# Kernel tuning notes

Measured on AMD Instinct MI355X. Metric: run time of the kernel, lower is better.

The kernel has to match this reference:

```python
import jax, jax.numpy as jnp
import numpy as np

N = 50000
E = 800000
IN_DIM = 256
HID = 64
HEADS = 4
OUT_DIM = 32
NEG_SLOPE = 0.2


def gat_conv(x, edge_index, W, a_src, a_dst, bias, heads, out_ch, concat):
    """PyG-style GATConv (eval mode, add_self_loops=True).
    x: [N, F_in]; edge_index: [2, E'] with row0=src, row1=dst.
    W: [F_in, heads*out_ch]; a_src/a_dst: [heads, out_ch]; bias: [heads*out_ch] or [out_ch].
    """
    n = x.shape[0]
    # add self loops
    loops = jnp.arange(n, dtype=edge_index.dtype)
    src = jnp.concatenate([edge_index[0], loops])
    dst = jnp.concatenate([edge_index[1], loops])

    h = (x @ W).reshape(n, heads, out_ch)              # [N, H, C]
    alpha_s = jnp.einsum('nhc,hc->nh', h, a_src)       # [N, H]
    alpha_d = jnp.einsum('nhc,hc->nh', h, a_dst)       # [N, H]
    e = alpha_s[src] + alpha_d[dst]                    # [E', H]
    e = jnp.where(e >= 0, e, NEG_SLOPE * e)            # leaky_relu

    # segment softmax over incoming edges of each dst node
    m = jax.ops.segment_max(e, dst, num_segments=n)    # [N, H]
    ex = jnp.exp(e - m[dst])
    denom = jax.ops.segment_sum(ex, dst, num_segments=n)
    alpha = ex / (denom[dst] + 1e-16)                  # [E', H]

    msg = h[src] * alpha[:, :, None]                   # [E', H, C]
    out = jax.ops.segment_sum(msg, dst, num_segments=n)  # [N, H, C]
    out = out.reshape(n, heads * out_ch) if concat else out.mean(axis=1)
    return out + bias


def setup_inputs() -> dict:
    key = jax.random.key(0)
    ks = jax.random.split(key, 10)
    x = jax.random.normal(ks[0], (N, IN_DIM), dtype=jnp.float32)
    edge_index = jax.random.randint(ks[1], (2, E), 0, N, dtype=jnp.int32)
    s1 = 1.0 / np.sqrt(IN_DIM)
    s2 = 1.0 / np.sqrt(HEADS * HID)
    return {
        'x': x,
        'edge_index': edge_index,
        'W1': jax.random.normal(ks[2], (IN_DIM, HEADS * HID), dtype=jnp.float32) * s1,
        'a_src1': jax.random.normal(ks[3], (HEADS, HID), dtype=jnp.float32) * s2,
        'a_dst1': jax.random.normal(ks[4], (HEADS, HID), dtype=jnp.float32) * s2,
        'b1': jnp.zeros((HEADS * HID,), dtype=jnp.float32),
        'W2': jax.random.normal(ks[5], (HEADS * HID, OUT_DIM), dtype=jnp.float32) * s2,
        'a_src2': jax.random.normal(ks[6], (1, OUT_DIM), dtype=jnp.float32) * 0.125,
        'a_dst2': jax.random.normal(ks[7], (1, OUT_DIM), dtype=jnp.float32) * 0.125,
        'b2': jnp.zeros((OUT_DIM,), dtype=jnp.float32),
    }


def reference(x, edge_index, W1, a_src1, a_dst1, b1, W2, a_src2, a_dst2, b2):
    h = gat_conv(x, edge_index, W1, a_src1, a_dst1, b1, HEADS, HID, concat=True)
    h = jax.nn.elu(h)
    out = gat_conv(h, edge_index, W2, a_src2, a_dst2, b2, 1, OUT_DIM, concat=False)
    return out
```

## Files before the change

### kernel.cpp

```cpp
#include <hip/hip_runtime.h>

#define NEG_SLOPE 0.2f
#define CAP 64
#define LOG2E 1.44269504f

typedef short bf16x8 __attribute__((ext_vector_type(8)));
typedef float f32x4 __attribute__((ext_vector_type(4)));
typedef _Float16 half2v __attribute__((ext_vector_type(2)));
typedef _Float16 half4v __attribute__((ext_vector_type(4)));
typedef _Float16 half8v __attribute__((ext_vector_type(8)));

__device__ inline short bf16_rne(float x) {
    unsigned u = __float_as_uint(x);
    unsigned r = u + 0x7FFFu + ((u >> 16) & 1u);
    return (short)(r >> 16);
}

__device__ inline float fast_exp2(float x) {
#if __has_builtin(__builtin_amdgcn_exp2f)
    return __builtin_amdgcn_exp2f(x);
#else
    return exp2f(x);
#endif
}


__global__ void k_prepw(const float* __restrict__ W1, short* __restrict__ Wt,
                        const float* __restrict__ W2, _Float16* __restrict__ W2t,
                        int* __restrict__ cursor, int* __restrict__ col, int N) {
    int colc = blockIdx.x;
    int k = threadIdx.x;
    Wt[(size_t)colc * 256 + k] = bf16_rne(W1[(size_t)k * 256 + colc]);
    if (colc < 32) W2t[(size_t)colc * 256 + k] = (_Float16)W2[(size_t)k * 32 + colc];
    int gid = blockIdx.x * 256 + threadIdx.x;
    if (gid < N) {
        cursor[gid] = 1;
        col[(size_t)gid * CAP] = gid;
    }
}


__global__ __launch_bounds__(256) void k_gemm_scatter(
        const float* __restrict__ x, const short* __restrict__ Wt,
        const float* __restrict__ a_src, const float* __restrict__ a_dst,
        _Float16* __restrict__ h1, float* __restrict__ as1, float* __restrict__ ad1,
        int N, int nGemm,
        const int* __restrict__ srcI, const int* __restrict__ dstI,
        int* __restrict__ cursor, int* __restrict__ col, int E) {
    __shared__ short Ab[64 * 40];
    __shared__ short Bb[256 * 40];

    if ((int)blockIdx.x >= nGemm) {
        int i = ((int)blockIdx.x - nGemm) * 256 + threadIdx.x;
        if (i < E) {
            int d = dstI[i];
            int p = atomicAdd(&cursor[d], 1);
            if (p < CAP) col[(size_t)d * CAP + p] = srcI[i];
        }
        return;
    }

    const int tid = threadIdx.x;
    const int lane = tid & 63;
    const int wc = tid >> 6;
    const int row0 = blockIdx.x * 64;
    const int m15 = lane & 15, quad = lane >> 4;

    f32x4 acc[4][4] = {};

    const int arow = tid >> 2;
    const int akseg = (tid & 3) * 8;

    for (int k0 = 0; k0 < 256; k0 += 32) {
        {
            int row = row0 + arow;
            float vals[8];
            if (row < N) {
                float4 v0 = *(const float4*)(x + (size_t)row * 256 + k0 + akseg);
                float4 v1 = *(const float4*)(x + (size_t)row * 256 + k0 + akseg + 4);
                vals[0] = v0.x; vals[1] = v0.y; vals[2] = v0.z; vals[3] = v0.w;
                vals[4] = v1.x; vals[5] = v1.y; vals[6] = v1.z; vals[7] = v1.w;
            } else {
#pragma unroll
                for (int i = 0; i < 8; ++i) vals[i] = 0.f;
            }
            short buf[8];
#pragma unroll
            for (int i = 0; i < 8; ++i) buf[i] = bf16_rne(vals[i]);
            *(bf16x8*)&Ab[arow * 40 + akseg] = *(bf16x8*)&buf[0];
        }
        {
#pragma unroll
            for (int s = 0; s < 4; ++s)
                *(bf16x8*)&Bb[tid * 40 + s * 8] =
                    *(const bf16x8*)(Wt + (size_t)tid * 256 + k0 + s * 8);
        }
        __syncthreads();
        bf16x8 ab[4];
#pragma unroll
        for (int mt = 0; mt < 4; ++mt)
            ab[mt] = *(const bf16x8*)&Ab[(mt * 16 + m15) * 40 + quad * 8];
#pragma unroll
        for (int nt = 0; nt < 4; ++nt) {
            int nn = wc * 64 + nt * 16 + m15;
            bf16x8 bb = *(const bf16x8*)&Bb[nn * 40 + quad * 8];
#pragma unroll
            for (int mt = 0; mt < 4; ++mt)
                acc[mt][nt] = __builtin_amdgcn_mfma_f32_16x16x32_bf16(ab[mt], bb, acc[mt][nt], 0, 0, 0);
        }
        __syncthreads();
    }
    const int head = wc;
#pragma unroll
    for (int mt = 0; mt < 4; ++mt) {
        float va[4] = {0.f, 0.f, 0.f, 0.f};
        float vd[4] = {0.f, 0.f, 0.f, 0.f};
#pragma unroll
        for (int nt = 0; nt < 4; ++nt) {
            int colg = wc * 64 + nt * 16 + m15;
            float asv = a_src[colg];
            float adv = a_dst[colg];
#pragma unroll
            for (int r = 0; r < 4; ++r) {
                float accv = acc[mt][nt][r];
                int row = row0 + mt * 16 + quad * 4 + r;
                if (row < N) h1[(size_t)row * 256 + colg] = (_Float16)accv;
                va[r] = fmaf(accv, asv, va[r]);
                vd[r] = fmaf(accv, adv, vd[r]);
            }
        }
#pragma unroll
        for (int r = 0; r < 4; ++r) {
#pragma unroll
            for (int mq = 1; mq < 16; mq <<= 1) {
                va[r] += __shfl_xor(va[r], mq);
                vd[r] += __shfl_xor(vd[r], mq);
            }
            int row = row0 + mt * 16 + quad * 4 + r;
            if (m15 == 0 && row < N) {
                as1[(size_t)row * 4 + head] = va[r] * LOG2E;
                ad1[(size_t)row * 4 + head] = vd[r] * LOG2E;
            }
        }
    }
}


__global__ __launch_bounds__(256) void k_fuse1(
        const _Float16* __restrict__ h1, const float* __restrict__ as1,
        const float* __restrict__ ad1, const int* __restrict__ cursor,
        const int* __restrict__ col, const float* __restrict__ b1,
        const _Float16* __restrict__ W2t, const float* __restrict__ a_s2,
        const float* __restrict__ a_d2, _Float16* __restrict__ z,
        float* __restrict__ as2, float* __restrict__ ad2, int N) {
    __shared__ _Float16 W2s[32 * 264];
    __shared__ _Float16 h2s[4 * 256];
    const int tid = threadIdx.x;
    const int l = tid & 63;
    const int wave = tid >> 6;
    const int n = blockIdx.x * 4 + wave;

    for (int i8 = tid; i8 < 1024; i8 += 256) {
        int elem = i8 * 8;
        int row = elem >> 8, k = elem & 255;
        *(half8v*)&W2s[row * 264 + k] = *(const half8v*)(W2t + (size_t)row * 256 + k);
    }
    __syncthreads();
    if (n >= N) return;

    const int head = l >> 4;
    const int beg = n * CAP;
    int deg = __builtin_amdgcn_readfirstlane(cursor[n]);
    if (deg > CAP) deg = CAP;
    int colv = 0;
    if (l < deg) colv = col[beg + l];
    float adv = ad1[(size_t)n * 4 + head];

    f32x4 a0 = {}, a1 = {}, a2 = {}, a3 = {};
    float s0 = 0.f, s1 = 0.f, s2 = 0.f, s3 = 0.f;
    int j = 0;
    for (; j + 3 < deg; j += 4) {
        int c0 = __builtin_amdgcn_readlane(colv, j);
        int c1 = __builtin_amdgcn_readlane(colv, j + 1);
        int c2 = __builtin_amdgcn_readlane(colv, j + 2);
        int c3 = __builtin_amdgcn_readlane(colv, j + 3);
        float e0 = as1[(size_t)c0 * 4 + head] + adv;
        float e1 = as1[(size_t)c1 * 4 + head] + adv;
        float e2 = as1[(size_t)c2 * 4 + head] + adv;
        float e3 = as1[(size_t)c3 * 4 + head] + adv;
        e0 = fmaxf(e0, NEG_SLOPE * e0); e1 = fmaxf(e1, NEG_SLOPE * e1);
        e2 = fmaxf(e2, NEG_SLOPE * e2); e3 = fmaxf(e3, NEG_SLOPE * e3);
        float p0 = fast_exp2(e0), p1 = fast_exp2(e1);
        float p2 = fast_exp2(e2), p3 = fast_exp2(e3);
        half4v h0 = *((const half4v*)(h1 + (size_t)c0 * 256) + l);
        half4v hv1 = *((const half4v*)(h1 + (size_t)c1 * 256) + l);
        half4v h2 = *((const half4v*)(h1 + (size_t)c2 * 256) + l);
        half4v h3 = *((const half4v*)(h1 + (size_t)c3 * 256) + l);
        s0 += p0; s1 += p1; s2 += p2; s3 += p3;
        a0 += __builtin_convertvector(h0, f32x4) * p0;
        a1 += __builtin_convertvector(hv1, f32x4) * p1;
        a2 += __builtin_convertvector(h2, f32x4) * p2;
        a3 += __builtin_convertvector(h3, f32x4) * p3;
    }
    for (; j < deg; ++j) {
        int c0 = __builtin_amdgcn_readlane(colv, j);
        float e0 = as1[(size_t)c0 * 4 + head] + adv;
        e0 = fmaxf(e0, NEG_SLOPE * e0);
        float p0 = fast_exp2(e0);
        half4v h0 = *((const half4v*)(h1 + (size_t)c0 * 256) + l);
        s0 += p0;
        a0 += __builtin_convertvector(h0, f32x4) * p0;
    }
    f32x4 at = (a0 + a1) + (a2 + a3);
    float iv = 1.f / ((s0 + s1) + (s2 + s3) + 1e-16f);
    float4 bb = *(const float4*)(b1 + l * 4);
    float4 v;
    v.x = at[0] * iv + bb.x;
    v.y = at[1] * iv + bb.y;
    v.z = at[2] * iv + bb.z;
    v.w = at[3] * iv + bb.w;
    v.x = (v.x > 0.f) ? v.x : (__expf(v.x) - 1.f);
    v.y = (v.y > 0.f) ? v.y : (__expf(v.y) - 1.f);
    v.z = (v.z > 0.f) ? v.z : (__expf(v.z) - 1.f);
    v.w = (v.w > 0.f) ? v.w : (__expf(v.w) - 1.f);
    half4v hv;
    hv.x = (_Float16)v.x; hv.y = (_Float16)v.y; hv.z = (_Float16)v.z; hv.w = (_Float16)v.w;
    *((half4v*)(h2s + wave * 256) + l) = hv;

    int c = l & 31;
    int kh = (l >> 5) * 128;
    const _Float16* hrow = h2s + wave * 256 + kh;
    const _Float16* wrow = W2s + c * 264 + kh;
    float accz = 0.f;
#pragma unroll
    for (int k = 0; k < 128; k += 8) {
        half8v hz = *(const half8v*)(hrow + k);
        half8v wz = *(const half8v*)(wrow + k);
#if __has_builtin(__builtin_amdgcn_fdot2)
        accz = __builtin_amdgcn_fdot2(__builtin_shufflevector(hz, hz, 0, 1),
                                      __builtin_shufflevector(wz, wz, 0, 1), accz, false);
        accz = __builtin_amdgcn_fdot2(__builtin_shufflevector(hz, hz, 2, 3),
                                      __builtin_shufflevector(wz, wz, 2, 3), accz, false);
        accz = __builtin_amdgcn_fdot2(__builtin_shufflevector(hz, hz, 4, 5),
                                      __builtin_shufflevector(wz, wz, 4, 5), accz, false);
        accz = __builtin_amdgcn_fdot2(__builtin_shufflevector(hz, hz, 6, 7),
                                      __builtin_shufflevector(wz, wz, 6, 7), accz, false);
#else
        accz = fmaf((float)hz[0], (float)wz[0], accz);
        accz = fmaf((float)hz[1], (float)wz[1], accz);
        accz = fmaf((float)hz[2], (float)wz[2], accz);
        accz = fmaf((float)hz[3], (float)wz[3], accz);
        accz = fmaf((float)hz[4], (float)wz[4], accz);
        accz = fmaf((float)hz[5], (float)wz[5], accz);
        accz = fmaf((float)hz[6], (float)wz[6], accz);
        accz = fmaf((float)hz[7], (float)wz[7], accz);
#endif
    }
    accz += __shfl_xor(accz, 32);
    float za = accz * a_s2[c];
    float zd = accz * a_d2[c];
#pragma unroll
    for (int mq = 1; mq < 32; mq <<= 1) {
        za += __shfl_xor(za, mq);
        zd += __shfl_xor(zd, mq);
    }
    if (l < 32) z[(size_t)n * 32 + c] = (_Float16)accz;
    if (l == 0) {
        as2[n] = za * LOG2E;
        ad2[n] = zd * LOG2E;
    }
}


__global__ void k_gather2(const _Float16* __restrict__ z, const float* __restrict__ as2,
                          const float* __restrict__ ad2, const int* __restrict__ cursor,
                          const int* __restrict__ col, const float* __restrict__ b2,
                          float* __restrict__ out, int N) {
    int n = blockIdx.x * 4 + (threadIdx.x >> 6);
    if (n >= N) return;
    int l = threadIdx.x & 63;
    int eo = l >> 3;
    int cg = l & 7;
    int beg = n * CAP;
    int deg = __builtin_amdgcn_readfirstlane(cursor[n]);
    if (deg > CAP) deg = CAP;
    int colv = 0;
    if (l < deg) colv = col[beg + l];
    float adn = ad2[n];
    f32x4 acc = {};
    float s = 0.f;

    const int nst = (deg + 7) >> 3;
    int srcA = __shfl(colv, eo);
    float aA = as2[srcA];
    half4v zA = *((const half4v*)(z + (size_t)srcA * 32) + cg);
    for (int t = 0; t < nst; ++t) {
        int srcB = 0; float aB = 0.f; half4v zB = {};
        if (t + 1 < nst) {
            srcB = __shfl(colv, (t + 1) * 8 + eo);
            aB = as2[srcB];
            zB = *((const half4v*)(z + (size_t)srcB * 32) + cg);
        }
        float e = aA + adn;
        e = fmaxf(e, NEG_SLOPE * e);
        float p = (t * 8 + eo < deg) ? fast_exp2(e) : 0.f;
        s += p;
        acc += __builtin_convertvector(zA, f32x4) * p;
        srcA = srcB; aA = aB; zA = zB;
    }
    float ax = acc[0], ay = acc[1], az = acc[2], aw = acc[3];
#pragma unroll
    for (int mq = 8; mq < 64; mq <<= 1) {
        ax += __shfl_xor(ax, mq);
        ay += __shfl_xor(ay, mq);
        az += __shfl_xor(az, mq);
        aw += __shfl_xor(aw, mq);
        s += __shfl_xor(s, mq);
    }
    if (eo == 0) {
        float iv = 1.f / (s + 1e-16f);
        float4 bb = *(const float4*)(b2 + cg * 4);
        float4 v;
        v.x = ax * iv + bb.x;
        v.y = ay * iv + bb.y;
        v.z = az * iv + bb.z;
        v.w = aw * iv + bb.w;
        *(float4*)(out + (size_t)n * 32 + cg * 4) = v;
    }
}


extern "C" void kernel_launch(void* const* d_in, const int* in_sizes, int n_in,
                              void* d_out, int out_size, void* d_ws, size_t ws_size,
                              hipStream_t stream) {
    const float* x    = (const float*)d_in[0];
    const int*   ei   = (const int*)d_in[1];
    const float* W1   = (const float*)d_in[2];
    const float* a_s1 = (const float*)d_in[3];
    const float* a_d1 = (const float*)d_in[4];
    const float* b1   = (const float*)d_in[5];
    const float* W2   = (const float*)d_in[6];
    const float* a_s2 = (const float*)d_in[7];
    const float* a_d2 = (const float*)d_in[8];
    const float* b2   = (const float*)d_in[9];
    float* out = (float*)d_out;

    const int N = in_sizes[0] / 256;
    const int E = in_sizes[1] / 2;
    const int* srcIdx = ei;
    const int* dstIdx = ei + E;

    char* ws = (char*)d_ws;
    size_t off = 0;
    auto alloc = [&](size_t bytes) {
        void* p = ws + off;
        off += (bytes + 255) & ~(size_t)255;
        return p;
    };
    _Float16* h1   = (_Float16*)alloc((size_t)N * 256 * 2);
    _Float16* z    = (_Float16*)alloc((size_t)N * 32 * 2);
    float* as1    = (float*)alloc((size_t)N * 16);
    float* ad1    = (float*)alloc((size_t)N * 16);
    float* as2    = (float*)alloc((size_t)N * 4);
    float* ad2    = (float*)alloc((size_t)N * 4);
    short* Wt     = (short*)alloc((size_t)256 * 256 * 2);
    _Float16* W2t = (_Float16*)alloc((size_t)32 * 256 * 2);
    int*   cursor = (int*)alloc((size_t)N * 4);
    int*   col    = (int*)alloc((size_t)N * CAP * 4);

    k_prepw<<<256, 256, 0, stream>>>(W1, Wt, W2, W2t, cursor, col, N);

    const int nGemm = (N + 63) / 64;
    const int nScat = (E + 255) / 256;
    k_gemm_scatter<<<nGemm + nScat, 256, 0, stream>>>(
        x, Wt, a_s1, a_d1, h1, as1, ad1, N, nGemm, srcIdx, dstIdx, cursor, col, E);

    k_fuse1<<<(N + 3) / 4, 256, 0, stream>>>(h1, as1, ad1, cursor, col, b1, W2t,
                                             a_s2, a_d2, z, as2, ad2, N);

    k_gather2<<<(N + 3) / 4, 256, 0, stream>>>(z, as2, ad2, cursor, col, b2, out, N);
}
```

Baseline: 262.0 us.

## Split scatter from GEMM kernel and pad per-node atomic cursors to separate lines

Moves the edge-scatter CSR build out of the combined GEMM/scatter launch into its own kernel that runs before the first-layer GEMM. It also spaces each node's atomic cursor 16 ints (64 bytes) apart, so concurrent atomics on different destination nodes hit different cache lines instead of contending on shared ones. The cost is a larger, sparser cursor array that later kernels read with strided loads, plus an extra kernel launch and the loss of overlap between the scatter and GEMM work.

```diff
diff --git a/kernel.cpp b/kernel.cpp
--- a/kernel.cpp
+++ b/kernel.cpp
@@ -2,6 +2,7 @@
 
 #define NEG_SLOPE 0.2f
 #define CAP 64
+#define CSTRIDE 16
 #define LOG2E 1.44269504f
 
 typedef short bf16x8 __attribute__((ext_vector_type(8)));
@@ -34,32 +35,29 @@
     if (colc < 32) W2t[(size_t)colc * 256 + k] = (_Float16)W2[(size_t)k * 32 + colc];
     int gid = blockIdx.x * 256 + threadIdx.x;
     if (gid < N) {
-        cursor[gid] = 1;
+        cursor[(size_t)gid * CSTRIDE] = 1;
         col[(size_t)gid * CAP] = gid;
     }
 }
 
 
-__global__ __launch_bounds__(256) void k_gemm_scatter(
+__global__ void k_scatter(const int* __restrict__ src, const int* __restrict__ dst,
+                          int* cursor, int* col, int E) {
+    int i = blockIdx.x * 256 + threadIdx.x;
+    if (i < E) {
+        int d = dst[i];
+        int p = atomicAdd(&cursor[(size_t)d * CSTRIDE], 1);
+        if (p < CAP) col[(size_t)d * CAP + p] = src[i];
+    }
+}
+
+
+__global__ __launch_bounds__(256) void k_gemm1(
         const float* __restrict__ x, const short* __restrict__ Wt,
         const float* __restrict__ a_src, const float* __restrict__ a_dst,
-        _Float16* __restrict__ h1, float* __restrict__ as1, float* __restrict__ ad1,
-        int N, int nGemm,
-        const int* __restrict__ srcI, const int* __restrict__ dstI,
-        int* __restrict__ cursor, int* __restrict__ col, int E) {
+        _Float16* __restrict__ h1, float* __restrict__ as1, float* __restrict__ ad1, int N) {
     __shared__ short Ab[64 * 40];
     __shared__ short Bb[256 * 40];
-
-    if ((int)blockIdx.x >= nGemm) {
-        int i = ((int)blockIdx.x - nGemm) * 256 + threadIdx.x;
-        if (i < E) {
-            int d = dstI[i];
-            int p = atomicAdd(&cursor[d], 1);
-            if (p < CAP) col[(size_t)d * CAP + p] = srcI[i];
-        }
-        return;
-    }
-
     const int tid = threadIdx.x;
     const int lane = tid & 63;
     const int wc = tid >> 6;
@@ -170,7 +168,7 @@
 
     const int head = l >> 4;
     const int beg = n * CAP;
-    int deg = __builtin_amdgcn_readfirstlane(cursor[n]);
+    int deg = __builtin_amdgcn_readfirstlane(cursor[(size_t)n * CSTRIDE]);
     if (deg > CAP) deg = CAP;
     int colv = 0;
     if (l < deg) colv = col[beg + l];
@@ -282,7 +280,7 @@
     int eo = l >> 3;
     int cg = l & 7;
     int beg = n * CAP;
-    int deg = __builtin_amdgcn_readfirstlane(cursor[n]);
+    int deg = __builtin_amdgcn_readfirstlane(cursor[(size_t)n * CSTRIDE]);
     if (deg > CAP) deg = CAP;
     int colv = 0;
     if (l < deg) colv = col[beg + l];
@@ -365,15 +363,13 @@
     float* ad2    = (float*)alloc((size_t)N * 4);
     short* Wt     = (short*)alloc((size_t)256 * 256 * 2);
     _Float16* W2t = (_Float16*)alloc((size_t)32 * 256 * 2);
-    int*   cursor = (int*)alloc((size_t)N * 4);
+    int*   cursor = (int*)alloc((size_t)N * CSTRIDE * 4);
     int*   col    = (int*)alloc((size_t)N * CAP * 4);
 
     k_prepw<<<256, 256, 0, stream>>>(W1, Wt, W2, W2t, cursor, col, N);
-
-    const int nGemm = (N + 63) / 64;
-    const int nScat = (E + 255) / 256;
-    k_gemm_scatter<<<nGemm + nScat, 256, 0, stream>>>(
-        x, Wt, a_s1, a_d1, h1, as1, ad1, N, nGemm, srcIdx, dstIdx, cursor, col, E);
+    k_scatter<<<(E + 255) / 256, 256, 0, stream>>>(srcIdx, dstIdx, cursor, col, E);
+
+    k_gemm1<<<(N + 63) / 64, 256, 0, stream>>>(x, Wt, a_s1, a_d1, h1, as1, ad1, N);
 
     k_fuse1<<<(N + 3) / 4, 256, 0, stream>>>(h1, as1, ad1, cursor, col, b1, W2t,
                                              a_s2, a_d2, z, as2, ad2, N);
```

Result: no change. 266.6 us (+1.7%).

## Interleave edge scatter inside GEMM blocks, alternating before and after the GEMM

Applied to the files above, without the earlier changes.

Drops the separate scatter-only blocks. Each of the GEMM blocks now also handles a contiguous chunk of the edge list, with odd blocks scattering before the GEMM and even blocks after it. The goal is to overlap the atomic-heavy, latency-bound scatter with compute-bound MFMA work inside the same CUs and to shrink the grid. The cost is longer per-block runtimes, a strided loop over about 1000 edges per block, and register pressure shared between the two phases.

```diff
diff --git a/kernel.cpp b/kernel.cpp
--- a/kernel.cpp
+++ b/kernel.cpp
@@ -6,7 +6,6 @@
 
 typedef short bf16x8 __attribute__((ext_vector_type(8)));
 typedef float f32x4 __attribute__((ext_vector_type(4)));
-typedef _Float16 half2v __attribute__((ext_vector_type(2)));
 typedef _Float16 half4v __attribute__((ext_vector_type(4)));
 typedef _Float16 half8v __attribute__((ext_vector_type(8)));
 
@@ -40,30 +39,34 @@
 }
 
 
-__global__ __launch_bounds__(256) void k_gemm_scatter(
+__global__ __launch_bounds__(256) void k_gemm1_scatter(
         const float* __restrict__ x, const short* __restrict__ Wt,
         const float* __restrict__ a_src, const float* __restrict__ a_dst,
-        _Float16* __restrict__ h1, float* __restrict__ as1, float* __restrict__ ad1,
-        int N, int nGemm,
+        _Float16* __restrict__ h1, float* __restrict__ as1, float* __restrict__ ad1, int N,
         const int* __restrict__ srcI, const int* __restrict__ dstI,
         int* __restrict__ cursor, int* __restrict__ col, int E) {
     __shared__ short Ab[64 * 40];
     __shared__ short Bb[256 * 40];
-
-    if ((int)blockIdx.x >= nGemm) {
-        int i = ((int)blockIdx.x - nGemm) * 256 + threadIdx.x;
-        if (i < E) {
+    const int tid = threadIdx.x;
+    const int b = blockIdx.x;
+    const int nGemm = gridDim.x;
+
+    const int chunk = (E + nGemm - 1) / nGemm;
+    const int ss = b * chunk;
+    const int se = (ss + chunk < E) ? (ss + chunk) : E;
+    const bool scatterFirst = (b & 1);
+
+    if (scatterFirst) {
+        for (int i = ss + tid; i < se; i += 256) {
             int d = dstI[i];
             int p = atomicAdd(&cursor[d], 1);
             if (p < CAP) col[(size_t)d * CAP + p] = srcI[i];
         }
-        return;
-    }
-
-    const int tid = threadIdx.x;
+    }
+
     const int lane = tid & 63;
     const int wc = tid >> 6;
-    const int row0 = blockIdx.x * 64;
+    const int row0 = b * 64;
     const int m15 = lane & 15, quad = lane >> 4;
 
     f32x4 acc[4][4] = {};
@@ -141,6 +144,14 @@
                 as1[(size_t)row * 4 + head] = va[r] * LOG2E;
                 ad1[(size_t)row * 4 + head] = vd[r] * LOG2E;
             }
+        }
+    }
+
+    if (!scatterFirst) {
+        for (int i = ss + tid; i < se; i += 256) {
+            int d = dstI[i];
+            int p = atomicAdd(&cursor[d], 1);
+            if (p < CAP) col[(size_t)d * CAP + p] = srcI[i];
         }
     }
 }
@@ -371,9 +382,8 @@
     k_prepw<<<256, 256, 0, stream>>>(W1, Wt, W2, W2t, cursor, col, N);
 
     const int nGemm = (N + 63) / 64;
-    const int nScat = (E + 255) / 256;
-    k_gemm_scatter<<<nGemm + nScat, 256, 0, stream>>>(
-        x, Wt, a_s1, a_d1, h1, as1, ad1, N, nGemm, srcIdx, dstIdx, cursor, col, E);
+    k_gemm1_scatter<<<nGemm, 256, 0, stream>>>(x, Wt, a_s1, a_d1, h1, as1, ad1, N,
+                                               srcIdx, dstIdx, cursor, col, E);
 
     k_fuse1<<<(N + 3) / 4, 256, 0, stream>>>(h1, as1, ad1, cursor, col, b1, W2t,
                                              a_s2, a_d2, z, as2, ad2, N);
```

Result: faster. 249.3 us (-4.9%).
